# Kernel tuning notes

Hardware: AMD Instinct MI355X
Metric: run time of the kernel (lower is better)

The kernel has to match this reference:

```python
import jax, jax.numpy as jnp
import numpy as np

N = 100_000      # nodes
E = 1_600_000    # edges (before self-loops)
IN = 128         # in_dim
H = 4            # heads (layer 1)
C = 32           # hidden_dim (per-head channels)
ED = 16          # edge_dim
NEG_SLOPE = 0.2  # PyG GATConv default


def setup_inputs() -> dict:
    key = jax.random.key(0)
    ks = jax.random.split(key, 16)
    s = 0.05
    return {
        "x": jax.random.normal(ks[0], (N, IN), jnp.float32),
        "edge_index": jax.random.randint(ks[1], (2, E), 0, N, dtype=jnp.int32),
        "edge_attr": jax.random.normal(ks[2], (E, ED), jnp.float32),
        # layer 1 params (heads=H, concat=True)
        "W1": jax.random.normal(ks[3], (IN, H * C), jnp.float32) * s,
        "W1e": jax.random.normal(ks[4], (ED, H * C), jnp.float32) * s,
        "a1_src": jax.random.normal(ks[5], (H, C), jnp.float32) * s,
        "a1_dst": jax.random.normal(ks[6], (H, C), jnp.float32) * s,
        "a1_edge": jax.random.normal(ks[7], (H, C), jnp.float32) * s,
        "b1": jax.random.normal(ks[8], (H * C,), jnp.float32) * s,
        # layer 2 params (heads=1, concat=False)
        "W2": jax.random.normal(ks[9], (H * C, C), jnp.float32) * s,
        "W2e": jax.random.normal(ks[10], (ED, C), jnp.float32) * s,
        "a2_src": jax.random.normal(ks[11], (1, C), jnp.float32) * s,
        "a2_dst": jax.random.normal(ks[12], (1, C), jnp.float32) * s,
        "a2_edge": jax.random.normal(ks[13], (1, C), jnp.float32) * s,
        "b2": jax.random.normal(ks[14], (C,), jnp.float32) * s,
    }


def _add_self_loops(src, dst, edge_attr, n):
    # PyG GATConv: add_self_loops=True, fill_value='mean' -> self-loop edge_attr
    # is the mean of incoming edge attrs per target node.
    deg = jax.ops.segment_sum(jnp.ones_like(dst, jnp.float32), dst, num_segments=n)
    mean_attr = jax.ops.segment_sum(edge_attr, dst, num_segments=n) / jnp.maximum(deg, 1.0)[:, None]
    loop = jnp.arange(n, dtype=src.dtype)
    src2 = jnp.concatenate([src, loop])
    dst2 = jnp.concatenate([dst, loop])
    attr2 = jnp.concatenate([edge_attr, mean_attr], axis=0)
    return src2, dst2, attr2


def _gat_conv(x, src, dst, eattr, W, We, a_s, a_d, a_e, b, concat):
    n = x.shape[0]
    Hh, Cc = a_s.shape
    h = (x @ W).reshape(n, Hh, Cc)                # [N,H,C]
    he = (eattr @ We).reshape(-1, Hh, Cc)          # [E',H,C]
    al_s = jnp.sum(h * a_s, axis=-1)               # [N,H]
    al_d = jnp.sum(h * a_d, axis=-1)               # [N,H]
    al_e = jnp.sum(he * a_e, axis=-1)              # [E',H]
    e = jax.nn.leaky_relu(al_s[src] + al_d[dst] + al_e, NEG_SLOPE)  # [E',H]
    # segment softmax over destination node neighborhoods
    m = jax.ops.segment_max(e, dst, num_segments=n)                 # [N,H]
    p = jnp.exp(e - m[dst])
    z = jax.ops.segment_sum(p, dst, num_segments=n)                 # [N,H]
    alpha = p / z[dst]                                              # [E',H]
    out = jax.ops.segment_sum(alpha[:, :, None] * h[src], dst, num_segments=n)  # [N,H,C]
    if concat:
        out = out.reshape(n, Hh * Cc)
    else:
        out = out.mean(axis=1)
    return out + b, alpha


def reference(x, edge_index, edge_attr,
              W1, W1e, a1_src, a1_dst, a1_edge, b1,
              W2, W2e, a2_src, a2_dst, a2_edge, b2):
    n = x.shape[0]
    src, dst, eattr = _add_self_loops(edge_index[0], edge_index[1], edge_attr, n)
    h1, _ = _gat_conv(x, src, dst, eattr, W1, W1e, a1_src, a1_dst, a1_edge, b1, concat=True)
    h1 = jax.nn.elu(h1)
    # dropout p applied in training only; inference reference -> identity
    h2, alpha2 = _gat_conv(h1, src, dst, eattr, W2, W2e, a2_src, a2_dst, a2_edge, b2, concat=False)
    h2 = jax.nn.elu(h2)
    edge_index_sl = jnp.stack([src, dst])
    return h2, edge_index_sl, alpha2
```

## Files before the change

kernel.cpp:

```cpp
#include <hip/hip_runtime.h>

#define NN 100000
#define NE 1600000
#define NE2 1700000
#define OUT_EI 3200000
#define OUT_AL 6600000
#define SLOPE 0.2f
#define NB 391
#define EPB 6400
#define NBB 250
#define CAP 5120

typedef unsigned short u16;
typedef unsigned int u32;
typedef __bf16 bf16x8 __attribute__((ext_vector_type(8)));
typedef float f32x4 __attribute__((ext_vector_type(4)));
typedef u32 u32x4 __attribute__((ext_vector_type(4)));

__device__ __forceinline__ float bf2f(u16 u){ return __uint_as_float(((u32)u) << 16); }
__device__ __forceinline__ u16 f2bf(float f){
    u32 x = __float_as_uint(f);
    x += 0x7FFFu + ((x >> 16) & 1u);
    return (u16)(x >> 16);
}
__device__ __forceinline__ float eluf(float v){ return v > 0.f ? v : (__expf(v) - 1.f); }
__device__ __forceinline__ float lreluf(float v){ return fmaxf(v, SLOPE * v); }
__device__ __forceinline__ float sel4f(float a, float b, float c, float d, int s){
    float x = (s & 1) ? b : a;
    float y = (s & 1) ? d : c;
    return (s & 2) ? y : x;
}

__global__ __launch_bounds__(256) void k_ale(const float* __restrict__ eattr,
                                             const float* __restrict__ W1e, const float* __restrict__ a1e,
                                             const float* __restrict__ W2e, const float* __restrict__ a2e,
                                             u16* __restrict__ ale1, u16* __restrict__ ale2){
    __shared__ float sq1[64], sq2[16];
    int t = threadIdx.x;
    if (t < 64){
        int k = t >> 2, h = t & 3;
        float s = 0.f;
        #pragma unroll 8
        for (int c = 0; c < 32; c++) s += W1e[k * 128 + h * 32 + c] * a1e[h * 32 + c];
        sq1[t] = s;
    }
    if (t < 16){
        float s2 = 0.f;
        #pragma unroll 8
        for (int c = 0; c < 32; c++) s2 += W2e[t * 32 + c] * a2e[c];
        sq2[t] = s2;
    }
    __syncthreads();
    int gt = blockIdx.x * 256 + t;
    int e = gt >> 2, part = gt & 3;
    f32x4 av = ((const f32x4*)eattr)[(size_t)e * 4 + part];
    int j0 = part * 4;
    float p0 = 0, p1 = 0, p2 = 0, p3 = 0, p4 = 0;
    #pragma unroll
    for (int k = 0; k < 4; k++){
        float a = av[k]; int j = j0 + k;
        p0 += a * sq1[j * 4 + 0]; p1 += a * sq1[j * 4 + 1];
        p2 += a * sq1[j * 4 + 2]; p3 += a * sq1[j * 4 + 3];
        p4 += a * sq2[j];
    }
    #pragma unroll
    for (int m = 1; m < 4; m <<= 1){
        p0 += __shfl_xor(p0, m); p1 += __shfl_xor(p1, m);
        p2 += __shfl_xor(p2, m); p3 += __shfl_xor(p3, m); p4 += __shfl_xor(p4, m);
    }
    if (part == 0){
        ushort4 w; w.x = f2bf(p0); w.y = f2bf(p1); w.z = f2bf(p2); w.w = f2bf(p3);
        ((ushort4*)ale1)[e] = w;
        ale2[e] = f2bf(p4);
    }
}

__global__ __launch_bounds__(256) void k_bscatter(const int* __restrict__ ei, const u16* __restrict__ ale1,
                                                  const u16* __restrict__ ale2,
                                                  int* __restrict__ bcnt, u32* __restrict__ binsP,
                                                  uint2* __restrict__ binsA, u16* __restrict__ binsA2){
    __shared__ int cnt[NB];
    __shared__ int base[NB];
    __shared__ int sdst[EPB];
    int t = threadIdx.x;
    for (int i = t; i < NB; i += 256) cnt[i] = 0;
    __syncthreads();
    int e0 = blockIdx.x * EPB;
    for (int i = t; i < EPB; i += 256){
        int dv = ei[NE + e0 + i];
        sdst[i] = dv;
        atomicAdd(&cnt[dv >> 8], 1);
    }
    __syncthreads();
    for (int i = t; i < NB; i += 256){
        int c = cnt[i];
        base[i] = c ? atomicAdd(&bcnt[i], c) : 0;
        cnt[i] = 0;
    }
    __syncthreads();
    const uint2* a1 = (const uint2*)ale1;
    for (int i = t; i < EPB; i += 256){
        int e = e0 + i;
        int dst = sdst[i];
        int b = dst >> 8;
        int r = base[b] + atomicAdd(&cnt[b], 1);
        if (r < CAP){
            size_t pos = (size_t)b * CAP + r;
            binsP[pos] = ((u32)(dst & 255) << 24) | (u32)ei[e];
            binsA[pos] = a1[e];
            binsA2[pos] = ale2[e];
        }
    }
}

__global__ __launch_bounds__(256) void k_fscatter(const u32* __restrict__ binsP, const uint2* __restrict__ binsA,
                                                  const u16* __restrict__ binsA2, const int* __restrict__ bcnt,
                                                  int* __restrict__ offsets,
                                                  int* __restrict__ src32, uint2* __restrict__ ale1p,
                                                  u16* __restrict__ ale2p){
    __shared__ int sc[512];
    __shared__ int d[256];
    __shared__ int s[256];
    __shared__ int cur[256];
    int t = threadIdx.x, b = blockIdx.x;
    int v0 = (t < NB) ? bcnt[t] : 0;
    int v1 = (t + 256 < NB) ? bcnt[t + 256] : 0;
    sc[t] = v0; sc[t + 256] = v1;
    d[t] = 0;
    __syncthreads();
    #pragma unroll
    for (int dd = 1; dd < 512; dd <<= 1){
        int x0 = (t >= dd) ? sc[t - dd] : 0;
        int x1 = (t + 256 >= dd) ? sc[t + 256 - dd] : 0;
        __syncthreads();
        sc[t] += x0; sc[t + 256] += x1;
        __syncthreads();
    }
    int myCnt = bcnt[b];
    int myBase = sc[b] - myCnt;
    size_t bb = (size_t)b * CAP;
    for (int i = t; i < myCnt; i += 256)
        atomicAdd(&d[binsP[bb + i] >> 24], 1);
    __syncthreads();
    int dv = d[t];
    s[t] = dv; __syncthreads();
    #pragma unroll
    for (int dd = 1; dd < 256; dd <<= 1){
        int x = (t >= dd) ? s[t - dd] : 0;
        __syncthreads();
        s[t] += x;
        __syncthreads();
    }
    int n = b * 256 + t;
    int off = myBase + (s[t] - dv) + n;
    if (n < NN) offsets[n] = off;
    cur[t] = off + 1;
    if (b == 0 && t == 0) offsets[NN] = NE + NN;
    __syncthreads();
    for (int i = t; i < myCnt; i += 256){
        u32 p = binsP[bb + i];
        int pos = atomicAdd(&cur[p >> 24], 1);
        src32[pos] = (int)(p & 0xFFFFFFu);
        ale1p[pos] = binsA[bb + i];
        ale2p[pos] = binsA2[bb + i];
    }
}

__global__ __launch_bounds__(256) void k_gemm1(const float* __restrict__ x, const float* __restrict__ W,
                                               const float* __restrict__ a1s, const float* __restrict__ a1d,
                                               u16* __restrict__ h1,
                                               float* __restrict__ al_s, float* __restrict__ al_d){
    __shared__ __align__(16) u16 sW[128 * 136];
    int t = threadIdx.x;
    for (int i = t; i < 128 * 128; i += 256){
        int k = i >> 7, c = i & 127;
        sW[c * 136 + k] = f2bf(W[i]);
    }
    __syncthreads();
    int lane = t & 63, wave = t >> 6;
    int quad = lane >> 4, m16 = lane & 15;
    int rowA = blockIdx.x * 64 + wave * 16 + m16;
    bf16x8 afr[4];
    if (rowA < NN){
        const f32x4* xr = (const f32x4*)(x + (size_t)rowA * 128);
        #pragma unroll
        for (int kk = 0; kk < 4; kk++){
            f32x4 va = xr[kk * 8 + quad * 2];
            f32x4 vb = xr[kk * 8 + quad * 2 + 1];
            #pragma unroll
            for (int i2 = 0; i2 < 4; i2++){ afr[kk][i2] = (__bf16)va[i2]; afr[kk][4 + i2] = (__bf16)vb[i2]; }
        }
    } else {
        #pragma unroll
        for (int kk = 0; kk < 4; kk++)
            #pragma unroll
            for (int i2 = 0; i2 < 8; i2++) afr[kk][i2] = (__bf16)0.f;
    }
    int rowbase = blockIdx.x * 64 + wave * 16 + quad * 4;
    float vsA[4][4], vdA[4][4];
    #pragma unroll
    for (int r = 0; r < 4; r++)
        #pragma unroll
        for (int h = 0; h < 4; h++){ vsA[r][h] = 0.f; vdA[r][h] = 0.f; }
    #pragma unroll
    for (int nt = 0; nt < 8; nt++){
        f32x4 acc = (f32x4){0.f, 0.f, 0.f, 0.f};
        const u16* wp = &sW[(nt * 16 + m16) * 136 + quad * 8];
        #pragma unroll
        for (int kk = 0; kk < 4; kk++){
            bf16x8 bfr = *(const bf16x8*)(wp + kk * 32);
            acc = __builtin_amdgcn_mfma_f32_16x16x32_bf16(afr[kk], bfr, acc, 0, 0, 0);
        }
        int col = nt * 16 + m16;
        float cs = a1s[col], cd = a1d[col];
        const int h = nt >> 1;
        #pragma unroll
        for (int r = 0; r < 4; r++){
            vsA[r][h] += acc[r] * cs;
            vdA[r][h] += acc[r] * cd;
            int row = rowbase + r;
            if (row < NN) h1[(size_t)row * 128 + col] = f2bf(acc[r]);
        }
    }
    #pragma unroll
    for (int r = 0; r < 4; r++)
        #pragma unroll
        for (int h = 0; h < 4; h++)
            #pragma unroll
            for (int m = 1; m < 16; m <<= 1){
                vsA[r][h] += __shfl_xor(vsA[r][h], m);
                vdA[r][h] += __shfl_xor(vdA[r][h], m);
            }
    int rs = m16 >> 2, hs = m16 & 3;
    float s0 = sel4f(vsA[0][0], vsA[0][1], vsA[0][2], vsA[0][3], hs);
    float s1 = sel4f(vsA[1][0], vsA[1][1], vsA[1][2], vsA[1][3], hs);
    float s2 = sel4f(vsA[2][0], vsA[2][1], vsA[2][2], vsA[2][3], hs);
    float s3 = sel4f(vsA[3][0], vsA[3][1], vsA[3][2], vsA[3][3], hs);
    float d0 = sel4f(vdA[0][0], vdA[0][1], vdA[0][2], vdA[0][3], hs);
    float d1 = sel4f(vdA[1][0], vdA[1][1], vdA[1][2], vdA[1][3], hs);
    float d2 = sel4f(vdA[2][0], vdA[2][1], vdA[2][2], vdA[2][3], hs);
    float d3 = sel4f(vdA[3][0], vdA[3][1], vdA[3][2], vdA[3][3], hs);
    float souts = sel4f(s0, s1, s2, s3, rs);
    float soutd = sel4f(d0, d1, d2, d3, rs);
    int row = rowbase + rs;
    if (row < NN){
        al_s[row * 4 + hs] = souts;
        al_d[row * 4 + hs] = soutd;
    }
}

__global__ __launch_bounds__(256) void k_node1(const int* __restrict__ src32, const u16* __restrict__ ale1u,
                                               const int* __restrict__ offsets,
                                               const float* __restrict__ al_s, const float* __restrict__ al_d,
                                               const u16* __restrict__ h1, const float* __restrict__ b1,
                                               u16* __restrict__ h1b){
    int wave = threadIdx.x >> 6, lane = threadIdx.x & 63;
    int n = blockIdx.x * 4 + wave;
    int start = offsets[n], end = offsets[n + 1];
    int degr = end - start - 1;
    int g = lane >> 4, l = lane & 15, hq = l >> 2;
    float aldh = al_d[n * 4 + hq];
    const u32x4* h1v = (const u32x4*)h1;
    float acc[8];
    #pragma unroll
    for (int k = 0; k < 8; k++) acc[k] = 0.f;
    float z = 0.f, sa = 0.f;
    int i = start + 1 + g;
    int i1 = i + 4, i2 = i + 8;
    int src0 = (i  < end) ? __builtin_nontemporal_load(src32 + i)  : n;
    int src1 = (i1 < end) ? __builtin_nontemporal_load(src32 + i1) : n;
    float a0   = (i < end) ? bf2f(__builtin_nontemporal_load(ale1u + (size_t)i * 4 + hq)) : 0.f;
    float als0 = al_s[src0 * 4 + hq];
    u32x4 v0 = h1v[(size_t)src0 * 16 + l];
    while (i < end){
        int src2 = (i2 < end) ? __builtin_nontemporal_load(src32 + i2) : n;
        float a1v  = (i1 < end) ? bf2f(__builtin_nontemporal_load(ale1u + (size_t)i1 * 4 + hq)) : 0.f;
        float als1 = al_s[src1 * 4 + hq];
        u32x4 v1 = h1v[(size_t)src1 * 16 + l];
        float e = __expf(lreluf(als0 + aldh + a0));
        z += e; sa += a0;
        #pragma unroll
        for (int k = 0; k < 4; k++){
            acc[2 * k]     += e * bf2f((u16)(v0[k] & 0xFFFFu));
            acc[2 * k + 1] += e * bf2f((u16)(v0[k] >> 16));
        }
        i = i1; i1 = i2; i2 += 4;
        src1 = src2; a0 = a1v; als0 = als1; v0 = v1;
    }
    z += __shfl_xor(z, 16); z += __shfl_xor(z, 32);
    sa += __shfl_xor(sa, 16); sa += __shfl_xor(sa, 32);
    float inv_deg = 1.f / fmaxf((float)degr, 1.f);
    float ps = __expf(lreluf(al_s[n * 4 + hq] + aldh + sa * inv_deg));
    z += ps;
    if (g == 0){
        u32x4 v = h1v[(size_t)n * 16 + l];
        #pragma unroll
        for (int k = 0; k < 4; k++){
            acc[2 * k]     += ps * bf2f((u16)(v[k] & 0xFFFFu));
            acc[2 * k + 1] += ps * bf2f((u16)(v[k] >> 16));
        }
    }
    #pragma unroll
    for (int k = 0; k < 8; k++){
        acc[k] += __shfl_xor(acc[k], 16);
        acc[k] += __shfl_xor(acc[k], 32);
    }
    if (g == 0){
        float rz = 1.f / z;
        u32x4 w;
        #pragma unroll
        for (int k = 0; k < 4; k++){
            float v0e = eluf(acc[2 * k]     * rz + b1[l * 8 + 2 * k]);
            float v1e = eluf(acc[2 * k + 1] * rz + b1[l * 8 + 2 * k + 1]);
            w[k] = (u32)f2bf(v0e) | ((u32)f2bf(v1e) << 16);
        }
        ((u32x4*)h1b)[(size_t)n * 16 + l] = w;
    }
}

__global__ __launch_bounds__(256) void k_gemm2(const u16* __restrict__ hin, const float* __restrict__ W,
                                               const float* __restrict__ a2s, const float* __restrict__ a2d,
                                               float* __restrict__ h2a,
                                               float* __restrict__ al_s, float* __restrict__ al_d){
    __shared__ __align__(16) u16 sW[32 * 136];
    int t = threadIdx.x;
    for (int i = t; i < 128 * 32; i += 256){
        int k = i >> 5, c = i & 31;
        sW[c * 136 + k] = f2bf(W[i]);
    }
    __syncthreads();
    int lane = t & 63, wave = t >> 6;
    int quad = lane >> 4, m16 = lane & 15;
    int rowA = blockIdx.x * 64 + wave * 16 + m16;
    bf16x8 afr[4];
    if (rowA < NN){
        const u16* xr = hin + (size_t)rowA * 128 + quad * 8;
        #pragma unroll
        for (int kk = 0; kk < 4; kk++) afr[kk] = *(const bf16x8*)(xr + kk * 32);
    } else {
        #pragma unroll
        for (int kk = 0; kk < 4; kk++)
            #pragma unroll
            for (int i2 = 0; i2 < 8; i2++) afr[kk][i2] = (__bf16)0.f;
    }
    int rowbase = blockIdx.x * 64 + wave * 16 + quad * 4;
    float vs2[4], vd2[4];
    #pragma unroll
    for (int r = 0; r < 4; r++){ vs2[r] = 0.f; vd2[r] = 0.f; }
    #pragma unroll
    for (int nt = 0; nt < 2; nt++){
        f32x4 acc = (f32x4){0.f, 0.f, 0.f, 0.f};
        const u16* wp = &sW[(nt * 16 + m16) * 136 + quad * 8];
        #pragma unroll
        for (int kk = 0; kk < 4; kk++){
            bf16x8 bfr = *(const bf16x8*)(wp + kk * 32);
            acc = __builtin_amdgcn_mfma_f32_16x16x32_bf16(afr[kk], bfr, acc, 0, 0, 0);
        }
        int col = nt * 16 + m16;
        float cs = a2s[col], cd = a2d[col];
        #pragma unroll
        for (int r = 0; r < 4; r++){
            vs2[r] += acc[r] * cs;
            vd2[r] += acc[r] * cd;
            int row = rowbase + r;
            if (row < NN) h2a[(size_t)row * 32 + col] = acc[r];
        }
    }
    #pragma unroll
    for (int r = 0; r < 4; r++)
        #pragma unroll
        for (int m = 1; m < 16; m <<= 1){
            vs2[r] += __shfl_xor(vs2[r], m);
            vd2[r] += __shfl_xor(vd2[r], m);
        }
    if (m16 < 4){
        int row = rowbase + m16;
        if (row < NN){
            al_s[row] = sel4f(vs2[0], vs2[1], vs2[2], vs2[3], m16);
            al_d[row] = sel4f(vd2[0], vd2[1], vd2[2], vd2[3], m16);
        }
    }
}

__global__ __launch_bounds__(256) void k_node2(const int* __restrict__ src32, const u16* __restrict__ ale2p,
                                               const int* __restrict__ offsets,
                                               const float* __restrict__ al_s, const float* __restrict__ al_d,
                                               const float* __restrict__ h2a, const float* __restrict__ b2,
                                               float* __restrict__ dout, float* __restrict__ rzv){
    int wave = threadIdx.x >> 6, lane = threadIdx.x & 63;
    int n = blockIdx.x * 4 + wave;
    int start = offsets[n], end = offsets[n + 1];
    int degr = end - start - 1;
    float aldn = al_d[n];
    int g = lane >> 3, l = lane & 7;
    const f32x4* h2v = (const f32x4*)h2a;
    f32x4 acc = (f32x4){0.f, 0.f, 0.f, 0.f};
    float z = 0.f, sa = 0.f;
    int i = start + 1 + g;
    int i1 = i + 8, i2 = i + 16;
    int src0 = (i  < end) ? __builtin_nontemporal_load(src32 + i)  : n;
    int src1 = (i1 < end) ? __builtin_nontemporal_load(src32 + i1) : n;
    float a0   = (i < end) ? bf2f(__builtin_nontemporal_load(ale2p + i)) : 0.f;
    float als0 = al_s[src0];
    f32x4 v0 = h2v[(size_t)src0 * 8 + l];
    while (i < end){
        int src2 = (i2 < end) ? __builtin_nontemporal_load(src32 + i2) : n;
        float a1v  = (i1 < end) ? bf2f(__builtin_nontemporal_load(ale2p + i1)) : 0.f;
        float als1 = al_s[src1];
        f32x4 v1 = h2v[(size_t)src1 * 8 + l];
        float e = __expf(lreluf(als0 + aldn + a0));
        z += e; sa += a0;
        #pragma unroll
        for (int k = 0; k < 4; k++) acc[k] += e * v0[k];
        i = i1; i1 = i2; i2 += 8;
        src1 = src2; a0 = a1v; als0 = als1; v0 = v1;
    }
    z += __shfl_xor(z, 8); z += __shfl_xor(z, 16); z += __shfl_xor(z, 32);
    sa += __shfl_xor(sa, 8); sa += __shfl_xor(sa, 16); sa += __shfl_xor(sa, 32);
    float mal = sa / fmaxf((float)degr, 1.f);
    float ps = __expf(lreluf(al_s[n] + aldn + mal));
    z += ps;
    float rz = 1.f / z;
    if (g == 0){
        f32x4 v = h2v[(size_t)n * 8 + l];
        #pragma unroll
        for (int k = 0; k < 4; k++) acc[k] += ps * v[k];
    }
    if (lane == 0){
        rzv[n] = rz;
        dout[OUT_AL + NE + n] = ps * rz;
        dout[OUT_EI + NE + n] = (float)n;
        dout[OUT_EI + NE2 + NE + n] = (float)n;
    }
    #pragma unroll
    for (int k = 0; k < 4; k++){
        acc[k] += __shfl_xor(acc[k], 8);
        acc[k] += __shfl_xor(acc[k], 16);
        acc[k] += __shfl_xor(acc[k], 32);
    }
    if (g == 0){
        f32x4 w;
        #pragma unroll
        for (int k = 0; k < 4; k++) w[k] = eluf(acc[k] + b2[l * 4 + k]);
        ((f32x4*)dout)[(size_t)n * 8 + l] = w;
    }
}

__global__ __launch_bounds__(256) void k_alpha(const int* __restrict__ ei, const u16* __restrict__ ale2,
                                               const float* __restrict__ al_s, const float* __restrict__ al_d,
                                               const float* __restrict__ rzv, float* __restrict__ dout){
    int e = blockIdx.x * 256 + threadIdx.x;
    int src = ei[e], dst = ei[NE + e];
    float a = bf2f(ale2[e]);
    float ev = __expf(lreluf(al_s[src] + al_d[dst] + a));
    __builtin_nontemporal_store(ev * rzv[dst], &dout[OUT_AL + e]);
    __builtin_nontemporal_store((float)src, &dout[OUT_EI + e]);
    __builtin_nontemporal_store((float)dst, &dout[OUT_EI + NE2 + e]);
}

extern "C" void kernel_launch(void* const* d_in, const int* in_sizes, int n_in,
                              void* d_out, int out_size, void* d_ws, size_t ws_size,
                              hipStream_t stream) {
    const float* x     = (const float*)d_in[0];
    const int*   ei    = (const int*)d_in[1];
    const float* eattr = (const float*)d_in[2];
    const float* W1    = (const float*)d_in[3];
    const float* W1e   = (const float*)d_in[4];
    const float* a1s   = (const float*)d_in[5];
    const float* a1d   = (const float*)d_in[6];
    const float* a1e   = (const float*)d_in[7];
    const float* b1    = (const float*)d_in[8];
    const float* W2    = (const float*)d_in[9];
    const float* W2e   = (const float*)d_in[10];
    const float* a2s   = (const float*)d_in[11];
    const float* a2d   = (const float*)d_in[12];
    const float* a2e   = (const float*)d_in[13];
    const float* b2    = (const float*)d_in[14];
    float* dout = (float*)d_out;

    char* ws = (char*)d_ws;
    size_t off = 0;
    auto alloc = [&](size_t bytes) -> void* {
        void* p = ws + off;
        off += (bytes + 255) & ~(size_t)255;
        return p;
    };
    int* bcnt = (int*)alloc((size_t)NB * 4);
    size_t zero_bytes = off;
    int*     offsets = (int*)alloc((size_t)(NN + 1) * 4);
    u32*     binsP   = (u32*)alloc((size_t)NB * CAP * 4);
    uint2*   binsA   = (uint2*)alloc((size_t)NB * CAP * 8);
    u16*     binsA2  = (u16*)alloc((size_t)NB * CAP * 2);
    int*     src32   = (int*)alloc((size_t)NE2 * 4);
    uint2*   ale1p   = (uint2*)alloc((size_t)NE2 * 8);
    u16*     ale2p   = (u16*)alloc((size_t)NE2 * 2);
    u16*     ale1    = (u16*)alloc((size_t)NE * 4 * 2);
    u16*     ale2    = (u16*)alloc((size_t)NE * 2);
    float*   al_s1   = (float*)alloc((size_t)NN * 4 * 4);
    float*   al_d1   = (float*)alloc((size_t)NN * 4 * 4);
    u16*     h1      = (u16*)alloc((size_t)NN * 128 * 2);
    u16*   h1b   = (u16*)binsP;
    char*  h1r   = (char*)h1;
    float* h2a   = (float*)(h1r);
    float* al_s2 = (float*)(h1r + 12800000);
    float* al_d2 = (float*)(h1r + 13200128);
    float* rzv   = (float*)(h1r + 13600256);

    const int TB = 256;
    hipMemsetAsync(d_ws, 0, zero_bytes, stream);

    k_ale<<<NE * 4 / TB, TB, 0, stream>>>(eattr, W1e, a1e, W2e, a2e, ale1, ale2);
    k_bscatter<<<NBB, TB, 0, stream>>>(ei, ale1, ale2, bcnt, binsP, binsA, binsA2);
    k_fscatter<<<NB, TB, 0, stream>>>(binsP, binsA, binsA2, bcnt, offsets, src32, ale1p, ale2p);
    k_gemm1<<<(NN + 63) / 64, TB, 0, stream>>>(x, W1, a1s, a1d, h1, al_s1, al_d1);
    k_node1<<<NN / 4, TB, 0, stream>>>(src32, (const u16*)ale1p, offsets, al_s1, al_d1, h1, b1, h1b);
    k_gemm2<<<(NN + 63) / 64, TB, 0, stream>>>(h1b, W2, a2s, a2d, h2a, al_s2, al_d2);
    k_node2<<<NN / 4, TB, 0, stream>>>(src32, ale2p, offsets, al_s2, al_d2, h2a, b2, dout, rzv);
    k_alpha<<<NE / TB, TB, 0, stream>>>(ei, ale2, al_s2, al_d2, rzv, dout);
}
```

Baseline: 594.0 us.

## Fuse layer-2 projection into node1 aggregation and store h2 as bf16

New measurement: 629.3 us. 6.0% more time.

```diff
diff --git a/kernel.cpp b/kernel.cpp
--- a/kernel.cpp
+++ b/kernel.cpp
@@ -10,6 +10,7 @@
 #define EPB 6400
 #define NBB 250
 #define CAP 5120
+#define NNP 100096
 
 typedef unsigned short u16;
 typedef unsigned int u32;
@@ -253,8 +254,16 @@
                                                const int* __restrict__ offsets,
                                                const float* __restrict__ al_s, const float* __restrict__ al_d,
                                                const u16* __restrict__ h1, const float* __restrict__ b1,
-                                               u16* __restrict__ h1b){
-    int wave = threadIdx.x >> 6, lane = threadIdx.x & 63;
+                                               const float* __restrict__ W2,
+                                               const float* __restrict__ a2s, const float* __restrict__ a2d,
+                                               u16* __restrict__ h2b,
+                                               float* __restrict__ al_s2, float* __restrict__ al_d2){
+    __shared__ float sW2[128 * 32];
+    __shared__ float sh1[4][128];
+    int t = threadIdx.x;
+    for (int i = t; i < 128 * 32; i += 256) sW2[i] = W2[i];
+    __syncthreads();
+    int wave = t >> 6, lane = t & 63;
     int n = blockIdx.x * 4 + wave;
     int start = offsets[n], end = offsets[n + 1];
     int degr = end - start - 1;
@@ -305,87 +314,39 @@
         acc[k] += __shfl_xor(acc[k], 16);
         acc[k] += __shfl_xor(acc[k], 32);
     }
-    if (g == 0){
-        float rz = 1.f / z;
-        u32x4 w;
+    float rz = 1.f / z;
+    if (lane < 16){
+        f32x4 w0, w1;
         #pragma unroll
         for (int k = 0; k < 4; k++){
-            float v0e = eluf(acc[2 * k]     * rz + b1[l * 8 + 2 * k]);
-            float v1e = eluf(acc[2 * k + 1] * rz + b1[l * 8 + 2 * k + 1]);
-            w[k] = (u32)f2bf(v0e) | ((u32)f2bf(v1e) << 16);
-        }
-        ((u32x4*)h1b)[(size_t)n * 16 + l] = w;
-    }
-}
-
-__global__ __launch_bounds__(256) void k_gemm2(const u16* __restrict__ hin, const float* __restrict__ W,
-                                               const float* __restrict__ a2s, const float* __restrict__ a2d,
-                                               float* __restrict__ h2a,
-                                               float* __restrict__ al_s, float* __restrict__ al_d){
-    __shared__ __align__(16) u16 sW[32 * 136];
-    int t = threadIdx.x;
-    for (int i = t; i < 128 * 32; i += 256){
-        int k = i >> 5, c = i & 31;
-        sW[c * 136 + k] = f2bf(W[i]);
-    }
-    __syncthreads();
-    int lane = t & 63, wave = t >> 6;
-    int quad = lane >> 4, m16 = lane & 15;
-    int rowA = blockIdx.x * 64 + wave * 16 + m16;
-    bf16x8 afr[4];
-    if (rowA < NN){
-        const u16* xr = hin + (size_t)rowA * 128 + quad * 8;
-        #pragma unroll
-        for (int kk = 0; kk < 4; kk++) afr[kk] = *(const bf16x8*)(xr + kk * 32);
-    } else {
-        #pragma unroll
-        for (int kk = 0; kk < 4; kk++)
-            #pragma unroll
-            for (int i2 = 0; i2 < 8; i2++) afr[kk][i2] = (__bf16)0.f;
-    }
-    int rowbase = blockIdx.x * 64 + wave * 16 + quad * 4;
-    float vs2[4], vd2[4];
-    #pragma unroll
-    for (int r = 0; r < 4; r++){ vs2[r] = 0.f; vd2[r] = 0.f; }
-    #pragma unroll
-    for (int nt = 0; nt < 2; nt++){
-        f32x4 acc = (f32x4){0.f, 0.f, 0.f, 0.f};
-        const u16* wp = &sW[(nt * 16 + m16) * 136 + quad * 8];
-        #pragma unroll
-        for (int kk = 0; kk < 4; kk++){
-            bf16x8 bfr = *(const bf16x8*)(wp + kk * 32);
-            acc = __builtin_amdgcn_mfma_f32_16x16x32_bf16(afr[kk], bfr, acc, 0, 0, 0);
-        }
-        int col = nt * 16 + m16;
-        float cs = a2s[col], cd = a2d[col];
-        #pragma unroll
-        for (int r = 0; r < 4; r++){
-            vs2[r] += acc[r] * cs;
-            vd2[r] += acc[r] * cd;
-            int row = rowbase + r;
-            if (row < NN) h2a[(size_t)row * 32 + col] = acc[r];
-        }
-    }
-    #pragma unroll
-    for (int r = 0; r < 4; r++)
-        #pragma unroll
-        for (int m = 1; m < 16; m <<= 1){
-            vs2[r] += __shfl_xor(vs2[r], m);
-            vd2[r] += __shfl_xor(vd2[r], m);
-        }
-    if (m16 < 4){
-        int row = rowbase + m16;
-        if (row < NN){
-            al_s[row] = sel4f(vs2[0], vs2[1], vs2[2], vs2[3], m16);
-            al_d[row] = sel4f(vd2[0], vd2[1], vd2[2], vd2[3], m16);
-        }
-    }
+            w0[k] = eluf(acc[k]     * rz + b1[l * 8 + k]);
+            w1[k] = eluf(acc[4 + k] * rz + b1[l * 8 + 4 + k]);
+        }
+        f32x4* dstp = (f32x4*)&sh1[wave][l * 8];
+        dstp[0] = w0; dstp[1] = w1;
+    }
+    int c = lane & 31, half = lane >> 5;
+    const float* hr = sh1[wave] + half * 64;
+    const float* wc = &sW2[half * 64 * 32 + c];
+    float s = 0.f;
+    #pragma unroll
+    for (int j = 0; j < 64; j += 4){
+        f32x4 rv = *(const f32x4*)(hr + j);
+        s += rv[0] * wc[(j + 0) * 32] + rv[1] * wc[(j + 1) * 32]
+           + rv[2] * wc[(j + 2) * 32] + rv[3] * wc[(j + 3) * 32];
+    }
+    s += __shfl_xor(s, 32);
+    if (half == 0) h2b[(size_t)n * 32 + c] = f2bf(s);
+    float vs = s * a2s[c], vd = s * a2d[c];
+    #pragma unroll
+    for (int m = 1; m < 32; m <<= 1){ vs += __shfl_xor(vs, m); vd += __shfl_xor(vd, m); }
+    if (lane == 0){ al_s2[n] = vs; al_d2[n] = vd; }
 }
 
 __global__ __launch_bounds__(256) void k_node2(const int* __restrict__ src32, const u16* __restrict__ ale2p,
                                                const int* __restrict__ offsets,
                                                const float* __restrict__ al_s, const float* __restrict__ al_d,
-                                               const float* __restrict__ h2a, const float* __restrict__ b2,
+                                               const u16* __restrict__ h2b, const float* __restrict__ b2,
                                                float* __restrict__ dout, float* __restrict__ rzv){
     int wave = threadIdx.x >> 6, lane = threadIdx.x & 63;
     int n = blockIdx.x * 4 + wave;
@@ -393,7 +354,7 @@
     int degr = end - start - 1;
     float aldn = al_d[n];
     int g = lane >> 3, l = lane & 7;
-    const f32x4* h2v = (const f32x4*)h2a;
+    const uint2* h2v = (const uint2*)h2b;
     f32x4 acc = (f32x4){0.f, 0.f, 0.f, 0.f};
     float z = 0.f, sa = 0.f;
     int i = start + 1 + g;
@@ -402,16 +363,18 @@
     int src1 = (i1 < end) ? __builtin_nontemporal_load(src32 + i1) : n;
     float a0   = (i < end) ? bf2f(__builtin_nontemporal_load(ale2p + i)) : 0.f;
     float als0 = al_s[src0];
-    f32x4 v0 = h2v[(size_t)src0 * 8 + l];
+    uint2 v0 = h2v[(size_t)src0 * 8 + l];
     while (i < end){
         int src2 = (i2 < end) ? __builtin_nontemporal_load(src32 + i2) : n;
         float a1v  = (i1 < end) ? bf2f(__builtin_nontemporal_load(ale2p + i1)) : 0.f;
         float als1 = al_s[src1];
-        f32x4 v1 = h2v[(size_t)src1 * 8 + l];
+        uint2 v1 = h2v[(size_t)src1 * 8 + l];
         float e = __expf(lreluf(als0 + aldn + a0));
         z += e; sa += a0;
-        #pragma unroll
-        for (int k = 0; k < 4; k++) acc[k] += e * v0[k];
+        acc[0] += e * bf2f((u16)(v0.x & 0xFFFFu));
+        acc[1] += e * bf2f((u16)(v0.x >> 16));
+        acc[2] += e * bf2f((u16)(v0.y & 0xFFFFu));
+        acc[3] += e * bf2f((u16)(v0.y >> 16));
         i = i1; i1 = i2; i2 += 8;
         src1 = src2; a0 = a1v; als0 = als1; v0 = v1;
     }
@@ -422,9 +385,11 @@
     z += ps;
     float rz = 1.f / z;
     if (g == 0){
-        f32x4 v = h2v[(size_t)n * 8 + l];
-        #pragma unroll
-        for (int k = 0; k < 4; k++) acc[k] += ps * v[k];
+        uint2 v = h2v[(size_t)n * 8 + l];
+        acc[0] += ps * bf2f((u16)(v.x & 0xFFFFu));
+        acc[1] += ps * bf2f((u16)(v.x >> 16));
+        acc[2] += ps * bf2f((u16)(v.y & 0xFFFFu));
+        acc[3] += ps * bf2f((u16)(v.y >> 16));
     }
     if (lane == 0){
         rzv[n] = rz;
@@ -441,7 +406,7 @@
     if (g == 0){
         f32x4 w;
         #pragma unroll
-        for (int k = 0; k < 4; k++) w[k] = eluf(acc[k] + b2[l * 4 + k]);
+        for (int k = 0; k < 4; k++) w[k] = eluf(acc[k] * rz + b2[l * 4 + k]);
         ((f32x4*)dout)[(size_t)n * 8 + l] = w;
     }
 }
@@ -499,12 +464,10 @@
     float*   al_s1   = (float*)alloc((size_t)NN * 4 * 4);
     float*   al_d1   = (float*)alloc((size_t)NN * 4 * 4);
     u16*     h1      = (u16*)alloc((size_t)NN * 128 * 2);
-    u16*   h1b   = (u16*)binsP;
-    char*  h1r   = (char*)h1;
-    float* h2a   = (float*)(h1r);
-    float* al_s2 = (float*)(h1r + 12800000);
-    float* al_d2 = (float*)(h1r + 13200128);
-    float* rzv   = (float*)(h1r + 13600256);
+    u16*   h2b   = (u16*)binsP;
+    float* al_s2 = (float*)binsA;
+    float* al_d2 = al_s2 + NNP;
+    float* rzv   = al_d2 + NNP;
 
     const int TB = 256;
     hipMemsetAsync(d_ws, 0, zero_bytes, stream);
@@ -513,8 +476,8 @@
     k_bscatter<<<NBB, TB, 0, stream>>>(ei, ale1, ale2, bcnt, binsP, binsA, binsA2);
     k_fscatter<<<NB, TB, 0, stream>>>(binsP, binsA, binsA2, bcnt, offsets, src32, ale1p, ale2p);
     k_gemm1<<<(NN + 63) / 64, TB, 0, stream>>>(x, W1, a1s, a1d, h1, al_s1, al_d1);
-    k_node1<<<NN / 4, TB, 0, stream>>>(src32, (const u16*)ale1p, offsets, al_s1, al_d1, h1, b1, h1b);
-    k_gemm2<<<(NN + 63) / 64, TB, 0, stream>>>(h1b, W2, a2s, a2d, h2a, al_s2, al_d2);
-    k_node2<<<NN / 4, TB, 0, stream>>>(src32, ale2p, offsets, al_s2, al_d2, h2a, b2, dout, rzv);
+    k_node1<<<NN / 4, TB, 0, stream>>>(src32, (const u16*)ale1p, offsets, al_s1, al_d1, h1, b1,
+                                       W2, a2s, a2d, h2b, al_s2, al_d2);
+    k_node2<<<NN / 4, TB, 0, stream>>>(src32, ale2p, offsets, al_s2, al_d2, h2b, b2, dout, rzv);
     k_alpha<<<NE / TB, TB, 0, stream>>>(ei, ale2, al_s2, al_d2, rzv, dout);
 }
```
